# Kernel tuning notes

Hardware: AMD Instinct MI355X
Metric: run time of the kernel (lower is better)

Reference implementation:

```python
import jax, jax.numpy as jnp
import numpy as np

B, N, H, E, C = 32, 128, 8, 64, 16
D = H * E  # d_model


def auto_head_configs(n_heads, patch_num):
    candidates = set()
    for d in range(1, patch_num + 1):
        for K in (3, 5, 7):
            eff = (K - 1) * d + 1
            if eff <= patch_num and K <= patch_num and (K % 2 == 1):
                candidates.add((K, d, eff))
    gk = patch_num if patch_num % 2 == 1 else patch_num - 1
    gk = max(1, gk)
    candidates.add((gk, 1, gk))
    candidates = sorted(candidates, key=lambda x: (x[2], -x[0], x[1]))
    if not candidates:
        return [(1, 1)] * n_heads
    configs = []
    for h in range(n_heads):
        idx = round(h * (len(candidates) - 1) / max(1, n_heads - 1))
        idx = min(idx, len(candidates) - 1)
        configs.append((candidates[idx][0], candidates[idx][1]))
    return configs


def build_na_mask(n_heads, patch_num):
    mask = np.zeros((n_heads, patch_num, patch_num), dtype=bool)
    for h, (K, d) in enumerate(auto_head_configs(n_heads, patch_num)):
        pos = np.arange(patch_num)[:, None]                      # [N,1]
        ideal = pos + (np.arange(K) - K // 2) * d                # [N,K]
        valid = (ideal >= 0) & (ideal < patch_num)
        rows = np.broadcast_to(pos, ideal.shape)
        mask[h, rows[valid], ideal[valid]] = True
    return mask


def setup_inputs() -> dict:
    key = jax.random.key(0)
    kq, kk, kv, k1, k2 = jax.random.split(key, 5)
    return {
        "queries": jax.random.normal(kq, (B, N, H, E), dtype=jnp.float32),
        "keys": jax.random.normal(kk, (B, C, N, H, E), dtype=jnp.float32),
        "values": jax.random.normal(kv, (B, C, N, H, E), dtype=jnp.float32),
        "w1": jax.random.normal(k1, (D, D // 4), dtype=jnp.float32) * 0.02,
        "b1": jnp.zeros((D // 4,), dtype=jnp.float32),
        "w2": jax.random.normal(k2, (D // 4, 1), dtype=jnp.float32) * 0.02,
        "b2": jnp.zeros((1,), dtype=jnp.float32),
        "na_mask": jnp.asarray(build_na_mask(H, N)),  # [H,N,N] bool
    }


def reference(queries, keys, values, w1, b1, w2, b2, na_mask):
    Bb, Nn, Hh, Ee = queries.shape
    Cc = keys.shape[1]
    scale = Ee ** (-0.5)
    # per-exo-variable gate from mean-pooled values
    v_pool = values.mean(axis=2).reshape(Bb, Cc, Hh * Ee)           # [B,C,D]
    hid = jax.nn.gelu(v_pool @ w1 + b1, approximate=False)
    gate = jax.nn.sigmoid(hid @ w2 + b2)                             # [B,C,1]
    q = queries.transpose(0, 2, 1, 3)                                # [B,H,N,E]
    k_cat = keys.transpose(0, 3, 1, 2, 4).reshape(Bb, Hh, Cc * Nn, Ee)
    v_g = values * gate[:, :, :, None, None]                         # [B,C,N,H,E]
    v_cat = v_g.transpose(0, 3, 1, 2, 4).reshape(Bb, Hh, Cc * Nn, Ee)
    # mask [H,N,N] -> [H,N,C*N] (same neighborhood replicated per exo var)
    tmask = jnp.broadcast_to(na_mask[:, :, None, :], (Hh, Nn, Cc, Nn)).reshape(Hh, Nn, Cc * Nn)
    attn = jnp.einsum('bhne,bhme->bhnm', q, k_cat) * scale
    attn = jnp.where(tmask, attn, -jnp.inf)
    attn = jax.nn.softmax(attn, axis=-1)
    out = jnp.einsum('bhnm,bhme->bhne', attn, v_cat)
    return out.transpose(0, 2, 1, 3)                                 # [B,N,H,E]
```

## Files before the change

### kernel.cpp

```cpp
#include <hip/hip_runtime.h>
#include <hip/hip_bf16.h>
#include <math.h>

#define BB 32
#define NN 128
#define HH 8
#define EE 64
#define CC 16
#define DD 512

#define NEG_BIG (-1.0e30f)

__device__ __forceinline__ float bf2f(unsigned short u) {
    union { unsigned int i; float f; } x; x.i = ((unsigned int)u) << 16; return x.f;
}
__device__ __forceinline__ float bflo(unsigned int u) {
    union { unsigned int i; float f; } x; x.i = u << 16; return x.f;
}
__device__ __forceinline__ float bfhi(unsigned int u) {
    union { unsigned int i; float f; } x; x.i = u & 0xffff0000u; return x.f;
}
__device__ __forceinline__ unsigned short f2bf(float f) {
    union { float f; unsigned int i; } x; x.f = f;
    unsigned int r = x.i + 0x7fffu + ((x.i >> 16) & 1u);
    return (unsigned short)(r >> 16);
}

template <bool F32>
__device__ __forceinline__ float ldx(const void* p, int i) {
    if constexpr (F32) return ((const float*)p)[i];
    else               return bf2f(((const unsigned short*)p)[i]);
}

__device__ const int g_dil[8] = {1, 5, 19, 14, 37, 23, 55, 63};

__global__ void detect_dtype(const unsigned short* __restrict__ q, int* __restrict__ flag) {
    const int lane = threadIdx.x;
    int outliers = 0;
    #pragma unroll
    for (int i = 0; i < 16; ++i) {
        unsigned short u = q[(i * 64 + lane) * 2];
        int e = (u >> 7) & 0xFF;
        int sane = (e >= 101 && e <= 140) || ((u & 0x7FFFu) == 0);
        outliers += !sane;
    }
    #pragma unroll
    for (int m = 32; m >= 1; m >>= 1) outliers += __shfl_xor(outliers, m, 64);
    if (lane == 0) *flag = (outliers > 256) ? 1 : 0;
}

template <bool F32>
__global__ __launch_bounds__(256) void gate_kernel(
    const void* __restrict__ values,
    const void* __restrict__ w1,
    const void* __restrict__ b1,
    const void* __restrict__ w2,
    const void* __restrict__ b2,
    const int*  __restrict__ flag,
    float* __restrict__ gate_out)
{
    if (*flag != (F32 ? 1 : 0)) return;
    __shared__ float vp[DD];
    __shared__ float hid[DD / 4];
    const int bc = blockIdx.x;
    const int t  = threadIdx.x;
    float a0 = 0.f, a1 = 0.f;
    if constexpr (F32) {
        const float2* vb = (const float2*)((const float*)values + (size_t)bc * NN * DD);
        #pragma unroll 4
        for (int n = 0; n < NN; ++n) { float2 u = vb[n * (DD / 2) + t]; a0 += u.x; a1 += u.y; }
    } else {
        const unsigned int* vb = (const unsigned int*)((const unsigned short*)values + (size_t)bc * NN * DD);
        #pragma unroll 4
        for (int n = 0; n < NN; ++n) { unsigned int u = vb[n * (DD / 2) + t]; a0 += bflo(u); a1 += bfhi(u); }
    }
    vp[2 * t]     = a0 * (1.0f / NN);
    vp[2 * t + 1] = a1 * (1.0f / NN);
    __syncthreads();
    if (t < DD / 4) {
        float a = ldx<F32>(b1, t);
        for (int dd = 0; dd < DD; ++dd)
            a += vp[dd] * ldx<F32>(w1, dd * (DD / 4) + t);
        hid[t] = 0.5f * a * (1.0f + erff(a * 0.70710678118654752440f));
    }
    __syncthreads();
    if (t < 64) {
        float s = hid[t] * ldx<F32>(w2, t) + hid[t + 64] * ldx<F32>(w2, t + 64);
        #pragma unroll
        for (int m = 32; m >= 1; m >>= 1) s += __shfl_xor(s, m, 64);
        if (t == 0) {
            float z = s + ldx<F32>(b2, 0);
            gate_out[bc] = 1.0f / (1.0f + expf(-z));
        }
    }
}

template <bool F32>
__global__ __launch_bounds__(256) void attn_kernel(
    const void* __restrict__ qptr,
    const void* __restrict__ kptr,
    const void* __restrict__ vptr,
    const float* __restrict__ gate,
    const int*  __restrict__ flag,
    void* __restrict__ optr)
{
    if (*flag != (F32 ? 1 : 0)) return;
    __shared__ float lds_w[4][CC * 5];
    const int tid  = threadIdx.x;
    const int wave = tid >> 6;
    const int lane = tid & 63;

    const int p    = blockIdx.x;
    const int virt = ((p & 7) << 10) | (p >> 3);
    const int gw   = virt * 4 + wave;
    const int n = gw & (NN - 1);
    const int h = (gw >> 7) & (HH - 1);
    const int b = gw >> 10;
    const int K   = ((h & 1) && (h != 7)) ? 5 : 3;
    const int dil = g_dil[h];
    const int nb  = CC * K;

    const int g   = lane >> 2;
    const int sub = lane & 3;

    const size_t qoff  = (((size_t)b * NN + n) * HH + h) * EE;
    const size_t kvoff = ((size_t)b * CC * NN) * DD + (size_t)h * EE;

    float qreg[16];
    if constexpr (F32) {
        const float4* qp = (const float4*)((const float*)qptr + qoff + sub * 16);
        #pragma unroll
        for (int i = 0; i < 4; ++i) {
            float4 u = qp[i];
            qreg[4 * i + 0] = u.x * 0.125f; qreg[4 * i + 1] = u.y * 0.125f;
            qreg[4 * i + 2] = u.z * 0.125f; qreg[4 * i + 3] = u.w * 0.125f;
        }
    } else {
        const uint4* qp = (const uint4*)((const unsigned short*)qptr + qoff + sub * 16);
        #pragma unroll
        for (int i = 0; i < 2; ++i) {
            uint4 u = qp[i];
            qreg[8 * i + 0] = bflo(u.x) * 0.125f; qreg[8 * i + 1] = bfhi(u.x) * 0.125f;
            qreg[8 * i + 2] = bflo(u.y) * 0.125f; qreg[8 * i + 3] = bfhi(u.y) * 0.125f;
            qreg[8 * i + 4] = bflo(u.z) * 0.125f; qreg[8 * i + 5] = bfhi(u.z) * 0.125f;
            qreg[8 * i + 6] = bflo(u.w) * 0.125f; qreg[8 * i + 7] = bfhi(u.w) * 0.125f;
        }
    }

    const size_t rowbase = kvoff + (size_t)g * NN * DD + (size_t)sub * 16;
    for (int k = 0; k < K; ++k) {
        int j = n + (k - (K >> 1)) * dil;
        float s = NEG_BIG;
        if (j >= 0 && j < NN) {
            size_t off = rowbase + (size_t)j * DD;
            float a0 = 0.f, a1 = 0.f, a2 = 0.f, a3 = 0.f;
            if constexpr (F32) {
                const float4* kp = (const float4*)((const float*)kptr + off);
                #pragma unroll
                for (int i = 0; i < 4; ++i) {
                    float4 kk = kp[i];
                    a0 += qreg[4 * i + 0] * kk.x; a1 += qreg[4 * i + 1] * kk.y;
                    a2 += qreg[4 * i + 2] * kk.z; a3 += qreg[4 * i + 3] * kk.w;
                }
            } else {
                const uint4* kp = (const uint4*)((const unsigned short*)kptr + off);
                #pragma unroll
                for (int i = 0; i < 2; ++i) {
                    uint4 kk = kp[i];
                    a0 += qreg[8 * i + 0] * bflo(kk.x); a1 += qreg[8 * i + 1] * bfhi(kk.x);
                    a2 += qreg[8 * i + 2] * bflo(kk.y); a3 += qreg[8 * i + 3] * bfhi(kk.y);
                    a0 += qreg[8 * i + 4] * bflo(kk.z); a1 += qreg[8 * i + 5] * bfhi(kk.z);
                    a2 += qreg[8 * i + 6] * bflo(kk.w); a3 += qreg[8 * i + 7] * bfhi(kk.w);
                }
            }
            s = (a0 + a1) + (a2 + a3);
            s += __shfl_xor(s, 1, 64);
            s += __shfl_xor(s, 2, 64);
        }
        if (sub == 0) lds_w[wave][k * CC + g] = s;
    }
    __syncthreads();

    float s0 = (lane < nb) ? lds_w[wave][lane] : NEG_BIG;
    float s1 = (nb > 64 && lane + 64 < nb) ? lds_w[wave][lane + 64] : NEG_BIG;
    float m = fmaxf(s0, s1);
    #pragma unroll
    for (int mm = 32; mm >= 1; mm >>= 1) m = fmaxf(m, __shfl_xor(m, mm, 64));
    float e0 = (s0 <= NEG_BIG) ? 0.f : expf(s0 - m);
    float e1 = (s1 <= NEG_BIG) ? 0.f : expf(s1 - m);
    float tsum = e0 + e1;
    #pragma unroll
    for (int mm = 32; mm >= 1; mm >>= 1) tsum += __shfl_xor(tsum, mm, 64);
    float inv = 1.0f / tsum;
    float gv  = gate[b * CC + (lane & 15)];
    lds_w[wave][lane] = e0 * inv * gv;
    if (nb > 64 && lane + 64 < nb)
        lds_w[wave][lane + 64] = e1 * inv * gv;
    __syncthreads();

    float acc0 = 0.f, acc1 = 0.f;
    for (int k = 0; k < K; ++k) {
        int j = n + (k - (K >> 1)) * dil;
        if (j < 0 || j >= NN) continue;
        const float* wrow = lds_w[wave] + k * CC;
        const size_t base = kvoff + (size_t)j * DD + lane;
        #pragma unroll
        for (int c = 0; c < CC; c += 2) {
            float w0 = wrow[c], w1 = wrow[c + 1];
            size_t o0 = base + (size_t)c * (NN * DD);
            size_t o1 = o0 + (size_t)(NN * DD);
            float v0 = F32 ? ((const float*)vptr)[o0] : bf2f(((const unsigned short*)vptr)[o0]);
            float v1 = F32 ? ((const float*)vptr)[o1] : bf2f(((const unsigned short*)vptr)[o1]);
            acc0 += w0 * v0;
            acc1 += w1 * v1;
        }
    }
    float acc = acc0 + acc1;
    if constexpr (F32) ((float*)optr)[qoff + lane] = acc;
    else               ((unsigned short*)optr)[qoff + lane] = f2bf(acc);
}

extern "C" void kernel_launch(void* const* d_in, const int* in_sizes, int n_in,
                              void* d_out, int out_size, void* d_ws, size_t ws_size,
                              hipStream_t stream) {
    const void* queries = d_in[0];
    const void* keys    = d_in[1];
    const void* values  = d_in[2];
    const void* w1      = d_in[3];
    const void* b1      = d_in[4];
    const void* w2      = d_in[5];
    const void* b2      = d_in[6];

    int*   flag    = (int*)d_ws;
    float* gate_ws = (float*)d_ws + 64;

    hipLaunchKernelGGL(detect_dtype, dim3(1), dim3(64), 0, stream,
                       (const unsigned short*)queries, flag);
    hipLaunchKernelGGL((gate_kernel<false>), dim3(BB * CC), dim3(256), 0, stream,
                       values, w1, b1, w2, b2, flag, gate_ws);
    hipLaunchKernelGGL((gate_kernel<true>), dim3(BB * CC), dim3(256), 0, stream,
                       values, w1, b1, w2, b2, flag, gate_ws);
    hipLaunchKernelGGL((attn_kernel<false>), dim3(BB * HH * NN / 4), dim3(256), 0, stream,
                       queries, keys, values, gate_ws, flag, d_out);
    hipLaunchKernelGGL((attn_kernel<true>), dim3(BB * HH * NN / 4), dim3(256), 0, stream,
                       queries, keys, values, gate_ws, flag, d_out);
}
```

Measured before the change: 346.8 us.

## Widen gate kernel parallelism, use wave-local syncs, vectorize value loads in attention

The gate kernel grows to 1024 threads: the mean pooling over N and the D×D/4 matvec are each split across four groups, with partial sums reduced through shared memory. In the attention kernel, the block-wide barriers become wave-local LDS waits, since each wave uses only its own lds_w slice. The QK loop becomes branchless by clamping invalid neighbour indices and masking the score afterwards. The PV loop now has each lane load two adjacent elements for half the channels, then combines the halves with a cross-lane shuffle, so loads are wider and per-iteration work is halved, at the cost of redundant loads for out-of-range neighbours.

```diff
diff --git a/kernel.cpp b/kernel.cpp
--- a/kernel.cpp
+++ b/kernel.cpp
@@ -32,6 +32,11 @@
     else               return bf2f(((const unsigned short*)p)[i]);
 }
 
+__device__ __forceinline__ void wave_lds_sync() {
+    asm volatile("s_waitcnt lgkmcnt(0)" ::: "memory");
+    __builtin_amdgcn_wave_barrier();
+}
+
 __device__ const int g_dil[8] = {1, 5, 19, 14, 37, 23, 55, 63};
 
 __global__ void detect_dtype(const unsigned short* __restrict__ q, int* __restrict__ flag) {
@@ -50,7 +55,7 @@
 }
 
 template <bool F32>
-__global__ __launch_bounds__(256) void gate_kernel(
+__global__ __launch_bounds__(1024) void gate_kernel(
     const void* __restrict__ values,
     const void* __restrict__ w1,
     const void* __restrict__ b1,
@@ -60,27 +65,48 @@
     float* __restrict__ gate_out)
 {
     if (*flag != (F32 ? 1 : 0)) return;
+    __shared__ float vps[4][DD];
     __shared__ float vp[DD];
+    __shared__ float hidp[4][DD / 4];
     __shared__ float hid[DD / 4];
-    const int bc = blockIdx.x;
-    const int t  = threadIdx.x;
+    const int bc  = blockIdx.x;
+    const int t   = threadIdx.x;
+    const int grp = t >> 8;
+    const int tt  = t & 255;
     float a0 = 0.f, a1 = 0.f;
     if constexpr (F32) {
-        const float2* vb = (const float2*)((const float*)values + (size_t)bc * NN * DD);
+        const float2* vb = (const float2*)((const float*)values + (size_t)bc * NN * DD)
+                           + (size_t)(grp * 32) * (DD / 2);
+        #pragma unroll 8
+        for (int n = 0; n < 32; ++n) { float2 u = vb[n * (DD / 2) + tt]; a0 += u.x; a1 += u.y; }
+    } else {
+        const unsigned int* vb = (const unsigned int*)((const unsigned short*)values + (size_t)bc * NN * DD)
+                                 + (size_t)(grp * 32) * (DD / 2);
+        #pragma unroll 8
+        for (int n = 0; n < 32; ++n) { unsigned int u = vb[n * (DD / 2) + tt]; a0 += bflo(u); a1 += bfhi(u); }
+    }
+    vps[grp][2 * tt]     = a0;
+    vps[grp][2 * tt + 1] = a1;
+    __syncthreads();
+    if (t < 256) {
+        float s0 = vps[0][2 * t]     + vps[1][2 * t]     + vps[2][2 * t]     + vps[3][2 * t];
+        float s1 = vps[0][2 * t + 1] + vps[1][2 * t + 1] + vps[2][2 * t + 1] + vps[3][2 * t + 1];
+        vp[2 * t]     = s0 * (1.0f / NN);
+        vp[2 * t + 1] = s1 * (1.0f / NN);
+    }
+    __syncthreads();
+    if (t < 512) {
+        const int o  = t & 127;
+        const int ch = t >> 7;
+        float a = 0.f;
         #pragma unroll 4
-        for (int n = 0; n < NN; ++n) { float2 u = vb[n * (DD / 2) + t]; a0 += u.x; a1 += u.y; }
-    } else {
-        const unsigned int* vb = (const unsigned int*)((const unsigned short*)values + (size_t)bc * NN * DD);
-        #pragma unroll 4
-        for (int n = 0; n < NN; ++n) { unsigned int u = vb[n * (DD / 2) + t]; a0 += bflo(u); a1 += bfhi(u); }
-    }
-    vp[2 * t]     = a0 * (1.0f / NN);
-    vp[2 * t + 1] = a1 * (1.0f / NN);
-    __syncthreads();
-    if (t < DD / 4) {
-        float a = ldx<F32>(b1, t);
-        for (int dd = 0; dd < DD; ++dd)
-            a += vp[dd] * ldx<F32>(w1, dd * (DD / 4) + t);
+        for (int dd = ch * 128; dd < ch * 128 + 128; ++dd)
+            a += vp[dd] * ldx<F32>(w1, dd * (DD / 4) + o);
+        hidp[ch][o] = a;
+    }
+    __syncthreads();
+    if (t < 128) {
+        float a = ldx<F32>(b1, t) + hidp[0][t] + hidp[1][t] + hidp[2][t] + hidp[3][t];
         hid[t] = 0.5f * a * (1.0f + erff(a * 0.70710678118654752440f));
     }
     __syncthreads();
@@ -148,38 +174,39 @@
     }
 
     const size_t rowbase = kvoff + (size_t)g * NN * DD + (size_t)sub * 16;
+    #pragma unroll 5
     for (int k = 0; k < K; ++k) {
-        int j = n + (k - (K >> 1)) * dil;
-        float s = NEG_BIG;
-        if (j >= 0 && j < NN) {
-            size_t off = rowbase + (size_t)j * DD;
-            float a0 = 0.f, a1 = 0.f, a2 = 0.f, a3 = 0.f;
-            if constexpr (F32) {
-                const float4* kp = (const float4*)((const float*)kptr + off);
-                #pragma unroll
-                for (int i = 0; i < 4; ++i) {
-                    float4 kk = kp[i];
-                    a0 += qreg[4 * i + 0] * kk.x; a1 += qreg[4 * i + 1] * kk.y;
-                    a2 += qreg[4 * i + 2] * kk.z; a3 += qreg[4 * i + 3] * kk.w;
-                }
-            } else {
-                const uint4* kp = (const uint4*)((const unsigned short*)kptr + off);
-                #pragma unroll
-                for (int i = 0; i < 2; ++i) {
-                    uint4 kk = kp[i];
-                    a0 += qreg[8 * i + 0] * bflo(kk.x); a1 += qreg[8 * i + 1] * bfhi(kk.x);
-                    a2 += qreg[8 * i + 2] * bflo(kk.y); a3 += qreg[8 * i + 3] * bfhi(kk.y);
-                    a0 += qreg[8 * i + 4] * bflo(kk.z); a1 += qreg[8 * i + 5] * bfhi(kk.z);
-                    a2 += qreg[8 * i + 6] * bflo(kk.w); a3 += qreg[8 * i + 7] * bfhi(kk.w);
-                }
+        int jr = n + (k - (K >> 1)) * dil;
+        bool valid = (jr >= 0) && (jr < NN);
+        int j = valid ? jr : n;
+        size_t off = rowbase + (size_t)j * DD;
+        float a0 = 0.f, a1 = 0.f, a2 = 0.f, a3 = 0.f;
+        if constexpr (F32) {
+            const float4* kp = (const float4*)((const float*)kptr + off);
+            #pragma unroll
+            for (int i = 0; i < 4; ++i) {
+                float4 kk = kp[i];
+                a0 += qreg[4 * i + 0] * kk.x; a1 += qreg[4 * i + 1] * kk.y;
+                a2 += qreg[4 * i + 2] * kk.z; a3 += qreg[4 * i + 3] * kk.w;
             }
-            s = (a0 + a1) + (a2 + a3);
-            s += __shfl_xor(s, 1, 64);
-            s += __shfl_xor(s, 2, 64);
-        }
+        } else {
+            const uint4* kp = (const uint4*)((const unsigned short*)kptr + off);
+            #pragma unroll
+            for (int i = 0; i < 2; ++i) {
+                uint4 kk = kp[i];
+                a0 += qreg[8 * i + 0] * bflo(kk.x); a1 += qreg[8 * i + 1] * bfhi(kk.x);
+                a2 += qreg[8 * i + 2] * bflo(kk.y); a3 += qreg[8 * i + 3] * bfhi(kk.y);
+                a0 += qreg[8 * i + 4] * bflo(kk.z); a1 += qreg[8 * i + 5] * bfhi(kk.z);
+                a2 += qreg[8 * i + 6] * bflo(kk.w); a3 += qreg[8 * i + 7] * bfhi(kk.w);
+            }
+        }
+        float s = (a0 + a1) + (a2 + a3);
+        s += __shfl_xor(s, 1, 64);
+        s += __shfl_xor(s, 2, 64);
+        s = valid ? s : NEG_BIG;
         if (sub == 0) lds_w[wave][k * CC + g] = s;
     }
-    __syncthreads();
+    wave_lds_sync();
 
     float s0 = (lane < nb) ? lds_w[wave][lane] : NEG_BIG;
     float s1 = (nb > 64 && lane + 64 < nb) ? lds_w[wave][lane + 64] : NEG_BIG;
@@ -196,28 +223,42 @@
     lds_w[wave][lane] = e0 * inv * gv;
     if (nb > 64 && lane + 64 < nb)
         lds_w[wave][lane + 64] = e1 * inv * gv;
-    __syncthreads();
-
+    wave_lds_sync();
+
+    const int e2   = lane & 31;
+    const int cpar = lane >> 5;
     float acc0 = 0.f, acc1 = 0.f;
+    #pragma unroll 5
     for (int k = 0; k < K; ++k) {
-        int j = n + (k - (K >> 1)) * dil;
-        if (j < 0 || j >= NN) continue;
+        int jr = n + (k - (K >> 1)) * dil;
+        int j = (jr >= 0 && jr < NN) ? jr : n;
         const float* wrow = lds_w[wave] + k * CC;
-        const size_t base = kvoff + (size_t)j * DD + lane;
-        #pragma unroll
-        for (int c = 0; c < CC; c += 2) {
-            float w0 = wrow[c], w1 = wrow[c + 1];
-            size_t o0 = base + (size_t)c * (NN * DD);
-            size_t o1 = o0 + (size_t)(NN * DD);
-            float v0 = F32 ? ((const float*)vptr)[o0] : bf2f(((const unsigned short*)vptr)[o0]);
-            float v1 = F32 ? ((const float*)vptr)[o1] : bf2f(((const unsigned short*)vptr)[o1]);
-            acc0 += w0 * v0;
-            acc1 += w1 * v1;
-        }
-    }
-    float acc = acc0 + acc1;
-    if constexpr (F32) ((float*)optr)[qoff + lane] = acc;
-    else               ((unsigned short*)optr)[qoff + lane] = f2bf(acc);
+        const size_t rbase = kvoff + (size_t)j * DD + 2 * e2;
+        #pragma unroll
+        for (int cc2 = 0; cc2 < CC / 2; ++cc2) {
+            int c = 2 * cc2 + cpar;
+            float w = wrow[c];
+            size_t o = rbase + (size_t)c * (NN * DD);
+            if constexpr (F32) {
+                const float2 v = *(const float2*)((const float*)vptr + o);
+                acc0 += w * v.x; acc1 += w * v.y;
+            } else {
+                unsigned int v = *(const unsigned int*)((const unsigned short*)vptr + o);
+                acc0 += w * bflo(v); acc1 += w * bfhi(v);
+            }
+        }
+    }
+    acc0 += __shfl_xor(acc0, 32, 64);
+    acc1 += __shfl_xor(acc1, 32, 64);
+    if (lane < 32) {
+        if constexpr (F32) {
+            float2 r; r.x = acc0; r.y = acc1;
+            ((float2*)((float*)optr + qoff))[e2] = r;
+        } else {
+            unsigned int pk = ((unsigned int)f2bf(acc1) << 16) | (unsigned int)f2bf(acc0);
+            ((unsigned int*)((unsigned short*)optr + qoff))[e2] = pk;
+        }
+    }
 }
 
 extern "C" void kernel_launch(void* const* d_in, const int* in_sizes, int n_in,
@@ -236,9 +277,9 @@
 
     hipLaunchKernelGGL(detect_dtype, dim3(1), dim3(64), 0, stream,
                        (const unsigned short*)queries, flag);
-    hipLaunchKernelGGL((gate_kernel<false>), dim3(BB * CC), dim3(256), 0, stream,
+    hipLaunchKernelGGL((gate_kernel<false>), dim3(BB * CC), dim3(1024), 0, stream,
                        values, w1, b1, w2, b2, flag, gate_ws);
-    hipLaunchKernelGGL((gate_kernel<true>), dim3(BB * CC), dim3(256), 0, stream,
+    hipLaunchKernelGGL((gate_kernel<true>), dim3(BB * CC), dim3(1024), 0, stream,
                        values, w1, b1, w2, b2, flag, gate_ws);
     hipLaunchKernelGGL((attn_kernel<false>), dim3(BB * HH * NN / 4), dim3(256), 0, stream,
                        queries, keys, values, gate_ws, flag, d_out);
```

New measurement: 363.6 us. 1.05x slower.
